# Performance work log

Hardware: AMD Instinct MI355X
Metric: run time of the kernel (lower is better)

Reference implementation:

```python
import jax, jax.numpy as jnp
import numpy as np

B, T, D = 2, 2048, 1024
HD = 128          # head_dim
NH = 16           # num_attention_heads
NKV = 8           # num_key_value_heads
EPS = 1e-6
ROPE_THETA = 1000000.0


def setup_inputs() -> dict:
    key = jax.random.key(0)
    ks = jax.random.split(key, 7)
    s = 0.02
    return {
        "x": jax.random.normal(ks[0], (B, T, D), dtype=jnp.float32),
        "wq": jax.random.normal(ks[1], (D, NH * HD), dtype=jnp.float32) * s,
        "wk": jax.random.normal(ks[2], (D, NKV * HD), dtype=jnp.float32) * s,
        "wv": jax.random.normal(ks[3], (D, NKV * HD), dtype=jnp.float32) * s,
        "wo": jax.random.normal(ks[4], (NH * HD, D), dtype=jnp.float32) * s,
        "q_norm_w": jnp.ones((HD,), dtype=jnp.float32),
        "k_norm_w": jnp.ones((HD,), dtype=jnp.float32),
    }


def _rms_norm(x, w):
    # torch source: x / (rms + eps) * w  (eps added OUTSIDE the sqrt)
    rms = jnp.sqrt(jnp.mean(x * x, axis=-1, keepdims=True))
    return w * (x / (rms + EPS))


def _rope_cos_sin(seq_len):
    pos = jnp.arange(seq_len, dtype=jnp.float32)
    thetas = ROPE_THETA ** (-2.0 * jnp.arange(HD // 2, dtype=jnp.float32) / HD)
    freqs = pos[:, None] * thetas[None, :]            # [T, HD//2]
    return jnp.cos(freqs), jnp.sin(freqs)


def _apply_rope(x, cos, sin):
    # x: [B, H, T, HD]; interleaved complex pairs (view_as_complex layout)
    xr = x[..., 0::2]
    xi = x[..., 1::2]
    c = cos[None, None, :, :]
    s = sin[None, None, :, :]
    out_r = xr * c - xi * s
    out_i = xr * s + xi * c
    return jnp.stack([out_r, out_i], axis=-1).reshape(x.shape)


def reference(x, wq, wk, wv, wo, q_norm_w, k_norm_w):
    b, t, d = x.shape
    q = (x @ wq).reshape(b, t, NH, HD).transpose(0, 2, 1, 3)    # [B,NH,T,HD]
    k = (x @ wk).reshape(b, t, NKV, HD).transpose(0, 2, 1, 3)   # [B,NKV,T,HD]
    v = (x @ wv).reshape(b, t, NKV, HD).transpose(0, 2, 1, 3)

    q = _rms_norm(q, q_norm_w)
    k = _rms_norm(k, k_norm_w)

    rep = NH // NKV
    k = jnp.repeat(k, rep, axis=1)   # GQA expand -> [B,NH,T,HD]
    v = jnp.repeat(v, rep, axis=1)

    cos, sin = _rope_cos_sin(t)
    q = _apply_rope(q, cos, sin)
    k = _apply_rope(k, cos, sin)

    scale = 1.0 / jnp.sqrt(jnp.float32(HD))
    scores = jnp.einsum("bhqd,bhkd->bhqk", q, k) * scale        # [B,NH,T,T]
    mask = jnp.triu(jnp.full((t, t), -jnp.inf, dtype=scores.dtype), k=1)
    scores = scores + mask
    attn = jax.nn.softmax(scores.astype(jnp.float32), axis=-1).astype(q.dtype)
    y = jnp.einsum("bhqk,bhkd->bhqd", attn, v)                  # [B,NH,T,HD]
    y = y.transpose(0, 2, 1, 3).reshape(b, t, NH * HD)
    return y @ wo
```

## Files before the change

kernel.cpp:

```cpp
#include <hip/hip_runtime.h>
#include <hip/hip_bf16.h>
#include <cstdint>
#include <cstddef>

using bf16 = __hip_bfloat16;
using short8 = __attribute__((ext_vector_type(8))) short;
using f32x4  = __attribute__((ext_vector_type(4))) float;
using f32x16 = __attribute__((ext_vector_type(16))) float;

#define DEVI __device__ __forceinline__

DEVI void async_ld16(const void* g, void* l) {
  __builtin_amdgcn_global_load_lds(
      (const __attribute__((address_space(1))) unsigned int*)g,
      (__attribute__((address_space(3))) unsigned int*)l, 16, 0, 0);
}

DEVI unsigned int cvt_pk_bf16(float lo, float hi) {
  unsigned int r;
  asm("v_cvt_pk_bf16_f32 %0, %1, %2" : "=v"(r) : "v"(lo), "v"(hi));
  return r;
}

__global__ void cvt_f32_bf16(const float* __restrict__ in, bf16* __restrict__ out, int n4) {
  int i = blockIdx.x * blockDim.x + threadIdx.x;
  if (i >= n4) return;
  float4 v = ((const float4*)in)[i];
  union { bf16 h[4]; ushort4 u; } o;
  o.h[0] = __float2bfloat16(v.x);
  o.h[1] = __float2bfloat16(v.y);
  o.h[2] = __float2bfloat16(v.z);
  o.h[3] = __float2bfloat16(v.w);
  ((ushort4*)out)[i] = o.u;
}

__global__ __launch_bounds__(256) void transpose_cvt(
    const float* __restrict__ in, bf16* __restrict__ out, int K, int N) {
  __shared__ float tile[32][33];
  int n0 = blockIdx.x * 32, k0 = blockIdx.y * 32;
  int tx = threadIdx.x & 31, ty = threadIdx.x >> 5;
#pragma unroll
  for (int i = 0; i < 32; i += 8)
    tile[ty + i][tx] = in[(size_t)(k0 + ty + i) * N + n0 + tx];
  __syncthreads();
#pragma unroll
  for (int i = 0; i < 32; i += 8)
    out[(size_t)(n0 + ty + i) * K + k0 + tx] = __float2bfloat16(tile[tx][ty + i]);
}

__global__ __launch_bounds__(256) void transpose_cvt3(
    const float* __restrict__ wq, const float* __restrict__ wk,
    const float* __restrict__ wv, bf16* __restrict__ wt) {
  __shared__ float tile[32][33];
  int z = blockIdx.z;
  const float* src; int N, coff, roff;
  if (z < 2)       { src = wq; N = 2048; coff = z * 1024; roff = z * 1024; }
  else if (z == 2) { src = wk; N = 1024; coff = 0;        roff = 2048; }
  else             { src = wv; N = 1024; coff = 0;        roff = 3072; }
  int n0 = coff + blockIdx.x * 32, k0 = blockIdx.y * 32;
  int tx = threadIdx.x & 31, ty = threadIdx.x >> 5;
#pragma unroll
  for (int i = 0; i < 32; i += 8)
    tile[ty + i][tx] = src[(size_t)(k0 + ty + i) * N + n0 + tx];
  __syncthreads();
#pragma unroll
  for (int i = 0; i < 32; i += 8)
    wt[(size_t)(roff + blockIdx.x * 32 + ty + i) * 1024 + k0 + tx] =
        __float2bfloat16(tile[tx][ty + i]);
}

__global__ void rope_tab(float2* __restrict__ tab) {
  int t = blockIdx.x, i = threadIdx.x;
  float ex = -2.f * (float)i * (1.f / 128.f);
  float theta = exp2f(ex * 19.9315685693241741f);
  float f = (float)t * theta;
  float sv, cv;
  sincosf(f, &sv, &cv);
  tab[t * 64 + i] = make_float2(cv, sv);
}

__global__ __launch_bounds__(256, 2) void gemm_qkv(
    const bf16* __restrict__ A, const bf16* __restrict__ Bt,
    const float* __restrict__ qnw, const float* __restrict__ knw,
    const float2* __restrict__ tab,
    bf16* __restrict__ Qh, bf16* __restrict__ Kh, bf16* __restrict__ Vt) {
  __shared__ alignas(16) bf16 As[2][128 * 64];
  __shared__ alignas(16) bf16 Bs[2][128 * 64];
  const int tid = threadIdx.x, lane = tid & 63, w = tid >> 6;
  const int wm = w >> 1, wn = w & 1;
  const int bx = blockIdx.x;
  const int m0 = blockIdx.y * 128, n0 = bx * 128;
  const int K = 1024, nt = 16;
  f32x4 acc[4][4] = {};

  const int srow = lane >> 3;
  const int scb  = (lane & 7) * 16;

  auto stage = [&](int buf, int kt) {
#pragma unroll
    for (int i = 0; i < 4; i++) {
      int row = w * 32 + i * 8 + srow;
      int src_cb = scb ^ ((row & 7) << 4);
      async_ld16((const char*)(A  + (size_t)(m0 + row) * K + kt * 64) + src_cb,
                 (char*)As[buf] + w * 4096 + i * 1024);
      async_ld16((const char*)(Bt + (size_t)(n0 + row) * K + kt * 64) + src_cb,
                 (char*)Bs[buf] + w * 4096 + i * 1024);
    }
  };

  stage(0, 0);
  stage(1, 1);

  for (int kt = 0; kt < nt; ++kt) {
    const int buf = kt & 1;
    if (kt + 1 < nt) asm volatile("s_waitcnt vmcnt(8)" ::: "memory");
    else             asm volatile("s_waitcnt vmcnt(0)" ::: "memory");
    __builtin_amdgcn_s_barrier();
#pragma unroll
    for (int ks = 0; ks < 2; ks++) {
      short8 af[4], bfr[4];
#pragma unroll
      for (int mi = 0; mi < 4; mi++) {
        int row = wm * 64 + mi * 16 + (lane & 15);
        int cb = (ks * 64 + (lane >> 4) * 16) ^ ((row & 7) << 4);
        af[mi] = *(const short8*)((const char*)As[buf] + row * 128 + cb);
      }
#pragma unroll
      for (int ni = 0; ni < 4; ni++) {
        int row = wn * 64 + ni * 16 + (lane & 15);
        int cb = (ks * 64 + (lane >> 4) * 16) ^ ((row & 7) << 4);
        bfr[ni] = *(const short8*)((const char*)Bs[buf] + row * 128 + cb);
      }
#pragma unroll
      for (int mi = 0; mi < 4; mi++)
#pragma unroll
        for (int ni = 0; ni < 4; ni++)
          acc[mi][ni] = __builtin_amdgcn_mfma_f32_16x16x32_bf16(af[mi], bfr[ni], acc[mi][ni], 0, 0, 0);
    }
    __builtin_amdgcn_s_barrier();
    __builtin_amdgcn_sched_barrier(0);
    if (kt + 2 < nt) stage(buf, kt + 2);
  }

  const int b = m0 >> 11;

  if (bx < 24) {
    __syncthreads();
    float* ssb = (float*)As;
    float s[4][4];
#pragma unroll
    for (int mi = 0; mi < 4; mi++)
#pragma unroll
      for (int r = 0; r < 4; r++) {
        float v0 = acc[mi][0][r], v1 = acc[mi][1][r];
        float v2 = acc[mi][2][r], v3 = acc[mi][3][r];
        float t = v0 * v0 + v1 * v1 + v2 * v2 + v3 * v3;
        t += __shfl_xor(t, 1);
        t += __shfl_xor(t, 2);
        t += __shfl_xor(t, 4);
        t += __shfl_xor(t, 8);
        s[mi][r] = t;
      }
    if ((lane & 15) == 0) {
#pragma unroll
      for (int mi = 0; mi < 4; mi++)
#pragma unroll
        for (int r = 0; r < 4; r++)
          ssb[wn * 128 + wm * 64 + mi * 16 + (lane >> 4) * 4 + r] = s[mi][r];
    }
    __syncthreads();

    const int isQ = (bx < 16);
    const int h = isQ ? bx : bx - 16;
    const float* wnp = isQ ? qnw : knw;
    bf16* dst = isQ ? Qh : Kh;
    const int NHH = isQ ? 16 : 8;
    const float qs = isQ ? 0.12751744416163417f : 1.f;
    float wd[4];
#pragma unroll
    for (int ni = 0; ni < 4; ni++) wd[ni] = wnp[wn * 64 + ni * 16 + (lane & 15)];

#pragma unroll
    for (int mi = 0; mi < 4; mi++)
#pragma unroll
      for (int r = 0; r < 4; r++) {
        int rl = wm * 64 + mi * 16 + (lane >> 4) * 4 + r;
        float tot = ssb[rl] + ssb[128 + rl];
        float inv = qs / (sqrtf(tot * 0.0078125f) + 1e-6f);
        int t = (m0 + rl) & 2047;
        bf16* drow = dst + ((size_t)(b * NHH + h) * 2048 + t) * 128;
#pragma unroll
        for (int ni = 0; ni < 4; ni++) {
          int d = wn * 64 + ni * 16 + (lane & 15);
          float val = acc[mi][ni][r] * inv * wd[ni];
          float prt = __shfl_xor(val, 1);
          float2 cs = tab[t * 64 + (d >> 1)];
          float o = (d & 1) ? (prt * cs.y + val * cs.x)
                            : (val * cs.x - prt * cs.y);
          drow[d] = __float2bfloat16(o);
        }
      }
  } else {
    __syncthreads();
    bf16* vt = (bf16*)As;
    const int vh = bx - 24;
#pragma unroll
    for (int mi = 0; mi < 4; mi++)
#pragma unroll
      for (int ni = 0; ni < 4; ni++) {
        int d = wn * 64 + ni * 16 + (lane & 15);
        int tl = wm * 64 + mi * 16 + (lane >> 4) * 4;
        unsigned int p0 = cvt_pk_bf16(acc[mi][ni][0], acc[mi][ni][1]);
        unsigned int p1 = cvt_pk_bf16(acc[mi][ni][2], acc[mi][ni][3]);
        int byte = d * 256 + ((tl * 2) ^ ((d & 7) << 4));
        *(uint2*)((char*)vt + byte) = make_uint2(p0, p1);
      }
    __syncthreads();
    bf16* dstV = Vt + (size_t)(b * 8 + vh) * 128 * 2048 + (m0 & 2047);
#pragma unroll
    for (int i = 0; i < 8; i++) {
      int flat = tid + i * 256;
      int d = flat >> 4, g = flat & 15;
      short8 v = *(const short8*)((const char*)vt + d * 256 + ((g * 16) ^ ((d & 7) << 4)));
      *(short8*)(dstV + (size_t)d * 2048 + g * 8) = v;
    }
  }
}

__global__ __launch_bounds__(256, 2) void gemm_out(
    const bf16* __restrict__ A, const bf16* __restrict__ Bt,
    float* __restrict__ C, int M, int N, int K) {
  __shared__ alignas(16) bf16 As[2][128 * 64];
  __shared__ alignas(16) bf16 Bs[2][128 * 64];
  const int tid = threadIdx.x, lane = tid & 63, w = tid >> 6;
  const int wm = w >> 1, wn = w & 1;
  const int m0 = blockIdx.y * 128, n0 = blockIdx.x * 128;
  const int nt = K >> 6;
  f32x4 acc[4][4] = {};

  const int srow = lane >> 3;
  const int scb  = (lane & 7) * 16;

  auto stage = [&](int buf, int kt) {
#pragma unroll
    for (int i = 0; i < 4; i++) {
      int row = w * 32 + i * 8 + srow;
      int src_cb = scb ^ ((row & 7) << 4);
      async_ld16((const char*)(A  + (size_t)(m0 + row) * K + kt * 64) + src_cb,
                 (char*)As[buf] + w * 4096 + i * 1024);
      async_ld16((const char*)(Bt + (size_t)(n0 + row) * K + kt * 64) + src_cb,
                 (char*)Bs[buf] + w * 4096 + i * 1024);
    }
  };

  stage(0, 0);
  stage(1, 1);

  for (int kt = 0; kt < nt; ++kt) {
    const int buf = kt & 1;
    if (kt + 1 < nt) asm volatile("s_waitcnt vmcnt(8)" ::: "memory");
    else             asm volatile("s_waitcnt vmcnt(0)" ::: "memory");
    __builtin_amdgcn_s_barrier();
#pragma unroll
    for (int ks = 0; ks < 2; ks++) {
      short8 af[4], bfr[4];
#pragma unroll
      for (int mi = 0; mi < 4; mi++) {
        int row = wm * 64 + mi * 16 + (lane & 15);
        int cb = (ks * 64 + (lane >> 4) * 16) ^ ((row & 7) << 4);
        af[mi] = *(const short8*)((const char*)As[buf] + row * 128 + cb);
      }
#pragma unroll
      for (int ni = 0; ni < 4; ni++) {
        int row = wn * 64 + ni * 16 + (lane & 15);
        int cb = (ks * 64 + (lane >> 4) * 16) ^ ((row & 7) << 4);
        bfr[ni] = *(const short8*)((const char*)Bs[buf] + row * 128 + cb);
      }
#pragma unroll
      for (int mi = 0; mi < 4; mi++)
#pragma unroll
        for (int ni = 0; ni < 4; ni++)
          acc[mi][ni] = __builtin_amdgcn_mfma_f32_16x16x32_bf16(af[mi], bfr[ni], acc[mi][ni], 0, 0, 0);
    }
    __builtin_amdgcn_s_barrier();
    __builtin_amdgcn_sched_barrier(0);
    if (kt + 2 < nt) stage(buf, kt + 2);
  }

  const int c0 = n0 + wn * 64 + (lane & 15);
  const int r0 = m0 + wm * 64 + (lane >> 4) * 4;
#pragma unroll
  for (int mi = 0; mi < 4; mi++)
#pragma unroll
    for (int ni = 0; ni < 4; ni++)
#pragma unroll
      for (int r = 0; r < 4; r++)
        C[(size_t)(r0 + mi * 16 + r) * N + (c0 + ni * 16)] = acc[mi][ni][r];
}

__global__ __launch_bounds__(512, 1) void flash_attn10(
    const bf16* __restrict__ Qh, const bf16* __restrict__ Kh,
    const bf16* __restrict__ Vt, bf16* __restrict__ Y) {
  __shared__ alignas(16) bf16 KB[4][64 * 128];
  __shared__ alignas(16) bf16 VB[4][128 * 64];
  __shared__ float MLs[128][2];
  const int tid = threadIdx.x, lane = tid & 63, w = tid >> 6;
  const int hi = lane >> 5, lq = lane & 31;
  const int grp = w >> 2, wl = w & 3;

  const int g = blockIdx.x;
  const int bh = (g & 7) * 4 + ((g >> 3) & 3);
  const int p  = g >> 5;
  const int b = bh >> 4, h = bh & 15, kvh = h >> 1;

  const bf16* Qg = Qh + (size_t)(b * 16 + h) * 2048 * 128;
  const bf16* Kg = Kh + (size_t)(b * 8 + kvh) * 2048 * 128;
  const bf16* Vg = Vt + (size_t)(b * 8 + kvh) * 128 * 2048;

  short8 qf[8];
  f32x16 oacc[4];
  float m, l;
  int qw = 0, qg = 0;

  auto stage2 = [&](int set, int k0e) {
#pragma unroll
    for (int gb = 0; gb < 2; gb++) {
      const int k0 = k0e + gb * 64;
      char* kb = (char*)KB[set * 2 + gb];
      char* vb = (char*)VB[set * 2 + gb];
#pragma unroll
      for (int i = 0; i < 2; i++) {
        int c = w * 2 + i;
        {
          int row = c * 4 + (lane >> 4);
          int cb = ((lane & 15) * 16) ^ ((row & 7) << 4);
          async_ld16((const char*)Kg + (size_t)(k0 + row) * 256 + cb, kb + c * 1024);
        }
        {
          int row = c * 8 + (lane >> 3);
          int cb = ((lane & 7) * 16) ^ ((row & 7) << 4);
          async_ld16((const char*)Vg + (size_t)row * 4096 + (size_t)k0 * 2 + cb, vb + c * 1024);
        }
      }
    }
  };

  auto setupTile = [&](int q0) {
    qw = q0 + wl * 32;
    qg = qw + lq;
#pragma unroll
    for (int dc = 0; dc < 8; dc++)
      qf[dc] = *(const short8*)(Qg + (size_t)qg * 128 + dc * 16 + hi * 8);
#pragma unroll
    for (int dc = 0; dc < 4; dc++)
#pragma unroll
      for (int r = 0; r < 16; r++) oacc[dc][r] = 0.f;
    m = -1e30f;
    l = 0.f;
  };

  auto computeStep = [&](int bufI, int k0) {
    f32x16 st[2] = {};
#pragma unroll
    for (int kc = 0; kc < 2; kc++) {
      int row = kc * 32 + lq;
      int swz = (row & 7) << 4;
      const char* kbase = (const char*)KB[bufI] + row * 256;
#pragma unroll
      for (int dc = 0; dc < 8; dc++) {
        short8 kf = *(const short8*)(kbase + ((dc * 32 + hi * 16) ^ swz));
        st[kc] = __builtin_amdgcn_mfma_f32_32x32x16_bf16(kf, qf[dc], st[kc], 0, 0, 0);
      }
    }
    const bool msk = (k0 + 63 > qw);
    if (msk) {
#pragma unroll
      for (int kc = 0; kc < 2; kc++)
#pragma unroll
        for (int rr = 0; rr < 16; rr++) {
          int kg = k0 + kc * 32 + (rr & 3) + 8 * (rr >> 2) + 4 * hi;
          if (kg > qg) st[kc][rr] = -1e30f;
        }
    }
    float mx[16];
#pragma unroll
    for (int rr = 0; rr < 16; rr++) mx[rr] = fmaxf(st[0][rr], st[1][rr]);
#pragma unroll
    for (int off = 8; off >= 1; off >>= 1)
#pragma unroll
      for (int rr = 0; rr < 8; rr++)
        if (rr < off) mx[rr] = fmaxf(mx[rr], mx[rr + off]);
    float pm = fmaxf(mx[0], __shfl_xor(mx[0], 32));
    if (__any(pm > m + 8.f)) {
      float mnew = fmaxf(m, pm);
      float alpha = exp2f(m - mnew);
      m = mnew;
      l *= alpha;
      float al[16];
#pragma unroll
      for (int rr = 0; rr < 16; rr++)
        al[rr] = __shfl(alpha, (rr & 3) + 8 * (rr >> 2) + 4 * hi);
#pragma unroll
      for (int dc = 0; dc < 4; dc++)
#pragma unroll
        for (int rr = 0; rr < 16; rr++) oacc[dc][rr] *= al[rr];
    }
#pragma unroll
    for (int kc = 0; kc < 2; kc++)
#pragma unroll
      for (int rr = 0; rr < 16; rr++) st[kc][rr] = exp2f(st[kc][rr] - m);
    float sm[16];
#pragma unroll
    for (int rr = 0; rr < 16; rr++) sm[rr] = st[0][rr] + st[1][rr];
#pragma unroll
    for (int off = 8; off >= 1; off >>= 1)
#pragma unroll
      for (int rr = 0; rr < 8; rr++)
        if (rr < off) sm[rr] += sm[rr + off];
    l += sm[0] + __shfl_xor(sm[0], 32);
    short8 af[4];
#pragma unroll
    for (int kc = 0; kc < 2; kc++)
#pragma unroll
      for (int sb = 0; sb < 2; sb++) {
        int base = sb * 8;
        unsigned int a01 = cvt_pk_bf16(st[kc][base + 0], st[kc][base + 1]);
        unsigned int a23 = cvt_pk_bf16(st[kc][base + 2], st[kc][base + 3]);
        unsigned int b01 = cvt_pk_bf16(st[kc][base + 4], st[kc][base + 5]);
        unsigned int b23 = cvt_pk_bf16(st[kc][base + 6], st[kc][base + 7]);
        unsigned int xa01 = (unsigned int)__shfl_xor((int)a01, 32);
        unsigned int xa23 = (unsigned int)__shfl_xor((int)a23, 32);
        unsigned int xb01 = (unsigned int)__shfl_xor((int)b01, 32);
        unsigned int xb23 = (unsigned int)__shfl_xor((int)b23, 32);
        union { unsigned int u[4]; short8 s; } f;
        f.u[0] = hi ? xb01 : a01;
        f.u[1] = hi ? xb23 : a23;
        f.u[2] = hi ? b01 : xa01;
        f.u[3] = hi ? b23 : xa23;
        af[kc * 2 + sb] = f.s;
      }
#pragma unroll
    for (int dc = 0; dc < 4; dc++) {
      int row = dc * 32 + lq;
      int swz = (row & 7) << 4;
      const char* vbase = (const char*)VB[bufI] + row * 128;
#pragma unroll
      for (int ks = 0; ks < 4; ks++) {
        short8 vf = *(const short8*)(vbase + ((ks * 32 + hi * 16) ^ swz));
        oacc[dc] = __builtin_amdgcn_mfma_f32_32x32x16_bf16(af[ks], vf, oacc[dc], 0, 0, 0);
      }
    }
  };

  auto runRounds = [&](int n) {
    const int R = n >> 1;
    for (int r = 0; r < R; ++r) {
      asm volatile("s_waitcnt vmcnt(0)" ::: "memory");
      __builtin_amdgcn_s_barrier();
      if (r + 1 < R) stage2((r + 1) & 1, (2 * r + 2) * 64);
      __builtin_amdgcn_sched_barrier(0);
      const int s = 2 * r + grp, k0 = s * 64;
      const int bufI = (r & 1) * 2 + grp;
      if (k0 < qw + 32) computeStep(bufI, k0);
    }
  };

  auto writePartials = [&]() {
    float* base = (wl < 2) ? (float*)KB[2] : (float*)VB[2];
#pragma unroll
    for (int dc = 0; dc < 4; dc++)
#pragma unroll
      for (int rr = 0; rr < 16; rr++) {
        int q = (wl & 1) * 32 + (rr & 3) + 8 * (rr >> 2) + 4 * hi;
        base[q * 128 + dc * 32 + lq] = oacc[dc][rr];
      }
    if (lane < 32) {
      MLs[wl * 32 + lane][0] = m;
      MLs[wl * 32 + lane][1] = l;
    }
  };

  auto mergeAndY = [&](int q0) {
    float m1 = MLs[wl * 32 + lq][0], l1 = MLs[wl * 32 + lq][1];
    float mN = fmaxf(m, m1);
    float e0 = exp2f(m - mN), e1 = exp2f(m1 - mN);
    float lT = l * e0 + l1 * e1;
    float inv = 1.f / lT;
    float e0r[16], e1r[16], ivr[16];
#pragma unroll
    for (int rr = 0; rr < 16; rr++) {
      int src = (rr & 3) + 8 * (rr >> 2) + 4 * hi;
      e0r[rr] = __shfl(e0, src);
      e1r[rr] = __shfl(e1, src);
      ivr[rr] = __shfl(inv, src);
    }
    const float* base = (wl < 2) ? (const float*)KB[2] : (const float*)VB[2];
#pragma unroll
    for (int dc = 0; dc < 4; dc++)
#pragma unroll
      for (int rr = 0; rr < 16; rr++) {
        int q = (wl & 1) * 32 + (rr & 3) + 8 * (rr >> 2) + 4 * hi;
        float o1 = base[q * 128 + dc * 32 + lq];
        float oT = oacc[dc][rr] * e0r[rr] + o1 * e1r[rr];
        int t = q0 + wl * 32 + (rr & 3) + 8 * (rr >> 2) + 4 * hi;
        Y[(size_t)(b * 2048 + t) * 2048 + h * 128 + dc * 32 + lq] =
            __float2bfloat16(oT * ivr[rr]);
      }
  };

  const int jA = 15 - p, jB = p;
  const int q0A = jA * 128, nA = 2 * jA + 2;
  const int q0B = jB * 128, nB = 2 * jB + 2;

  setupTile(q0A);
  stage2(0, 0);
  runRounds(nA);
  __syncthreads();
  stage2(0, 0);
  if (grp == 1) writePartials();
  __syncthreads();
  if (grp == 0) mergeAndY(q0A);
  setupTile(q0B);
  runRounds(nB);
  __syncthreads();
  if (grp == 1) writePartials();
  __syncthreads();
  if (grp == 0) mergeAndY(q0B);
}

extern "C" void kernel_launch(void* const* d_in, const int* in_sizes, int n_in,
                              void* d_out, int out_size, void* d_ws, size_t ws_size,
                              hipStream_t stream) {
  (void)in_sizes; (void)n_in; (void)out_size; (void)ws_size;
  const float* x   = (const float*)d_in[0];
  const float* wq  = (const float*)d_in[1];
  const float* wk  = (const float*)d_in[2];
  const float* wv  = (const float*)d_in[3];
  const float* wo  = (const float*)d_in[4];
  const float* qnw = (const float*)d_in[5];
  const float* knw = (const float*)d_in[6];
  float* out = (float*)d_out;
  char* ws = (char*)d_ws;
  const size_t MB = 1u << 20;
  bf16*   xb  = (bf16*)(ws + 0 * MB);
  bf16*   wt  = (bf16*)(ws + 8 * MB);
  bf16*   wot = (bf16*)(ws + 16 * MB);
  float2* tab = (float2*)(ws + 52 * MB);
  bf16*   Qh  = (bf16*)(ws + 53 * MB);
  bf16*   Kh  = (bf16*)(ws + 69 * MB);
  bf16*   Vtr = (bf16*)(ws + 77 * MB);
  bf16*   Yb  = (bf16*)(ws + 85 * MB);

  cvt_f32_bf16<<<4096, 256, 0, stream>>>(x, xb, 1048576);
  transpose_cvt3<<<dim3(32, 32, 4), 256, 0, stream>>>(wq, wk, wv, wt);
  transpose_cvt<<<dim3(32, 64), 256, 0, stream>>>(wo, wot, 2048, 1024);
  rope_tab<<<2048, 64, 0, stream>>>(tab);
  gemm_qkv<<<dim3(32, 32), 256, 0, stream>>>(xb, wt, qnw, knw, tab, Qh, Kh, Vtr);
  flash_attn10<<<256, 512, 0, stream>>>(Qh, Kh, Vtr, Yb);
  gemm_out<<<dim3(8, 32), 256, 0, stream>>>(Yb, wot, out, 4096, 1024, 2048);
}
```

Baseline: 166.6 us.

## Merge prep kernels into one launch and shrink output GEMM M-tile to 64

The four preprocessing kernels (x conversion, QKV weight transpose, Wo transpose, rope table) are combined into a single launch that branches on block index, removing launch gaps between small kernels. The output projection GEMM now uses 64x128 tiles with each wave covering 64x32, doubling the grid from 256 to 512 blocks on the device and allowing three blocks per CU. This improves CU occupancy for the small output GEMM at the cost of more redundant B-tile loads and lower per-wave arithmetic intensity.

```diff
diff --git a/kernel.cpp b/kernel.cpp
--- a/kernel.cpp
+++ b/kernel.cpp
@@ -22,61 +22,55 @@
   return r;
 }
 
-__global__ void cvt_f32_bf16(const float* __restrict__ in, bf16* __restrict__ out, int n4) {
-  int i = blockIdx.x * blockDim.x + threadIdx.x;
-  if (i >= n4) return;
-  float4 v = ((const float4*)in)[i];
-  union { bf16 h[4]; ushort4 u; } o;
-  o.h[0] = __float2bfloat16(v.x);
-  o.h[1] = __float2bfloat16(v.y);
-  o.h[2] = __float2bfloat16(v.z);
-  o.h[3] = __float2bfloat16(v.w);
-  ((ushort4*)out)[i] = o.u;
-}
-
-__global__ __launch_bounds__(256) void transpose_cvt(
-    const float* __restrict__ in, bf16* __restrict__ out, int K, int N) {
-  __shared__ float tile[32][33];
-  int n0 = blockIdx.x * 32, k0 = blockIdx.y * 32;
-  int tx = threadIdx.x & 31, ty = threadIdx.x >> 5;
-#pragma unroll
-  for (int i = 0; i < 32; i += 8)
-    tile[ty + i][tx] = in[(size_t)(k0 + ty + i) * N + n0 + tx];
-  __syncthreads();
-#pragma unroll
-  for (int i = 0; i < 32; i += 8)
-    out[(size_t)(n0 + ty + i) * K + k0 + tx] = __float2bfloat16(tile[tx][ty + i]);
-}
-
-__global__ __launch_bounds__(256) void transpose_cvt3(
-    const float* __restrict__ wq, const float* __restrict__ wk,
-    const float* __restrict__ wv, bf16* __restrict__ wt) {
-  __shared__ float tile[32][33];
-  int z = blockIdx.z;
-  const float* src; int N, coff, roff;
-  if (z < 2)       { src = wq; N = 2048; coff = z * 1024; roff = z * 1024; }
-  else if (z == 2) { src = wk; N = 1024; coff = 0;        roff = 2048; }
-  else             { src = wv; N = 1024; coff = 0;        roff = 3072; }
-  int n0 = coff + blockIdx.x * 32, k0 = blockIdx.y * 32;
-  int tx = threadIdx.x & 31, ty = threadIdx.x >> 5;
-#pragma unroll
-  for (int i = 0; i < 32; i += 8)
-    tile[ty + i][tx] = src[(size_t)(k0 + ty + i) * N + n0 + tx];
-  __syncthreads();
-#pragma unroll
-  for (int i = 0; i < 32; i += 8)
-    wt[(size_t)(roff + blockIdx.x * 32 + ty + i) * 1024 + k0 + tx] =
-        __float2bfloat16(tile[tx][ty + i]);
-}
-
-__global__ void rope_tab(float2* __restrict__ tab) {
-  int t = blockIdx.x, i = threadIdx.x;
-  float ex = -2.f * (float)i * (1.f / 128.f);
-  float theta = exp2f(ex * 19.9315685693241741f);
-  float f = (float)t * theta;
-  float sv, cv;
-  sincosf(f, &sv, &cv);
-  tab[t * 64 + i] = make_float2(cv, sv);
+__global__ __launch_bounds__(256) void prep(
+    const float* __restrict__ x, const float* __restrict__ wq,
+    const float* __restrict__ wk, const float* __restrict__ wv,
+    const float* __restrict__ wo, bf16* __restrict__ xb,
+    bf16* __restrict__ wt, bf16* __restrict__ wot, float2* __restrict__ tab) {
+  const int z = blockIdx.x, tid = threadIdx.x;
+  if (z < 4096) {
+    int i = z * 256 + tid;
+    float4 v = ((const float4*)x)[i];
+    union { bf16 h[4]; ushort4 u; } o;
+    o.h[0] = __float2bfloat16(v.x);
+    o.h[1] = __float2bfloat16(v.y);
+    o.h[2] = __float2bfloat16(v.z);
+    o.h[3] = __float2bfloat16(v.w);
+    ((ushort4*)xb)[i] = o.u;
+  } else if (z < 10240) {
+    __shared__ float tile[32][33];
+    const float* src; bf16* dst; int N, K, n0, k0, roff;
+    if (z < 8192) {
+      int z2 = z - 4096;
+      int xb_ = z2 & 31, yb = (z2 >> 5) & 31, zz = z2 >> 10;
+      if (zz < 2)       { src = wq; N = 2048; n0 = zz * 1024 + xb_ * 32; roff = zz * 1024 + xb_ * 32; }
+      else if (zz == 2) { src = wk; N = 1024; n0 = xb_ * 32; roff = 2048 + xb_ * 32; }
+      else              { src = wv; N = 1024; n0 = xb_ * 32; roff = 3072 + xb_ * 32; }
+      K = 1024; k0 = yb * 32; dst = wt;
+    } else {
+      int z3 = z - 8192;
+      int xb_ = z3 & 31, yb = z3 >> 5;
+      src = wo; N = 1024; K = 2048; n0 = xb_ * 32; k0 = yb * 32; roff = xb_ * 32;
+      dst = wot;
+    }
+    int tx = tid & 31, ty = tid >> 5;
+#pragma unroll
+    for (int i = 0; i < 32; i += 8)
+      tile[ty + i][tx] = src[(size_t)(k0 + ty + i) * N + n0 + tx];
+    __syncthreads();
+#pragma unroll
+    for (int i = 0; i < 32; i += 8)
+      dst[(size_t)(roff + ty + i) * K + k0 + tx] = __float2bfloat16(tile[tx][ty + i]);
+  } else {
+    int z4 = z - 10240;
+    int t = z4 * 4 + (tid >> 6), i = tid & 63;
+    float ex = -2.f * (float)i * (1.f / 128.f);
+    float theta = exp2f(ex * 19.9315685693241741f);
+    float f = (float)t * theta;
+    float sv, cv;
+    sincosf(f, &sv, &cv);
+    tab[t * 64 + i] = make_float2(cv, sv);
+  }
 }
 
 __global__ __launch_bounds__(256, 2) void gemm_qkv(
@@ -227,29 +221,32 @@
   }
 }
 
-__global__ __launch_bounds__(256, 2) void gemm_out(
+__global__ __launch_bounds__(256, 3) void gemm_out64(
     const bf16* __restrict__ A, const bf16* __restrict__ Bt,
     float* __restrict__ C, int M, int N, int K) {
-  __shared__ alignas(16) bf16 As[2][128 * 64];
+  __shared__ alignas(16) bf16 As[2][64 * 64];
   __shared__ alignas(16) bf16 Bs[2][128 * 64];
   const int tid = threadIdx.x, lane = tid & 63, w = tid >> 6;
-  const int wm = w >> 1, wn = w & 1;
-  const int m0 = blockIdx.y * 128, n0 = blockIdx.x * 128;
+  const int m0 = blockIdx.y * 64, n0 = blockIdx.x * 128;
   const int nt = K >> 6;
-  f32x4 acc[4][4] = {};
-
-  const int srow = lane >> 3;
-  const int scb  = (lane & 7) * 16;
+  f32x4 acc[4][2] = {};
 
   auto stage = [&](int buf, int kt) {
 #pragma unroll
+    for (int i = 0; i < 2; i++) {
+      int c = tid + i * 256;
+      int row = c >> 3;
+      int cb = ((c & 7) * 16) ^ ((row & 7) << 4);
+      async_ld16((const char*)(A + (size_t)(m0 + row) * K + kt * 64) + cb,
+                 (char*)As[buf] + i * 4096 + tid * 16);
+    }
+#pragma unroll
     for (int i = 0; i < 4; i++) {
-      int row = w * 32 + i * 8 + srow;
-      int src_cb = scb ^ ((row & 7) << 4);
-      async_ld16((const char*)(A  + (size_t)(m0 + row) * K + kt * 64) + src_cb,
-                 (char*)As[buf] + w * 4096 + i * 1024);
-      async_ld16((const char*)(Bt + (size_t)(n0 + row) * K + kt * 64) + src_cb,
-                 (char*)Bs[buf] + w * 4096 + i * 1024);
+      int c = tid + i * 256;
+      int row = c >> 3;
+      int cb = ((c & 7) * 16) ^ ((row & 7) << 4);
+      async_ld16((const char*)(Bt + (size_t)(n0 + row) * K + kt * 64) + cb,
+                 (char*)Bs[buf] + i * 4096 + tid * 16);
     }
   };
 
@@ -258,28 +255,28 @@
 
   for (int kt = 0; kt < nt; ++kt) {
     const int buf = kt & 1;
-    if (kt + 1 < nt) asm volatile("s_waitcnt vmcnt(8)" ::: "memory");
+    if (kt + 1 < nt) asm volatile("s_waitcnt vmcnt(6)" ::: "memory");
     else             asm volatile("s_waitcnt vmcnt(0)" ::: "memory");
     __builtin_amdgcn_s_barrier();
 #pragma unroll
     for (int ks = 0; ks < 2; ks++) {
-      short8 af[4], bfr[4];
+      short8 af[4], bfr[2];
 #pragma unroll
       for (int mi = 0; mi < 4; mi++) {
-        int row = wm * 64 + mi * 16 + (lane & 15);
+        int row = mi * 16 + (lane & 15);
         int cb = (ks * 64 + (lane >> 4) * 16) ^ ((row & 7) << 4);
         af[mi] = *(const short8*)((const char*)As[buf] + row * 128 + cb);
       }
 #pragma unroll
-      for (int ni = 0; ni < 4; ni++) {
-        int row = wn * 64 + ni * 16 + (lane & 15);
+      for (int ni = 0; ni < 2; ni++) {
+        int row = w * 32 + ni * 16 + (lane & 15);
         int cb = (ks * 64 + (lane >> 4) * 16) ^ ((row & 7) << 4);
         bfr[ni] = *(const short8*)((const char*)Bs[buf] + row * 128 + cb);
       }
 #pragma unroll
       for (int mi = 0; mi < 4; mi++)
 #pragma unroll
-        for (int ni = 0; ni < 4; ni++)
+        for (int ni = 0; ni < 2; ni++)
           acc[mi][ni] = __builtin_amdgcn_mfma_f32_16x16x32_bf16(af[mi], bfr[ni], acc[mi][ni], 0, 0, 0);
     }
     __builtin_amdgcn_s_barrier();
@@ -287,12 +284,12 @@
     if (kt + 2 < nt) stage(buf, kt + 2);
   }
 
-  const int c0 = n0 + wn * 64 + (lane & 15);
-  const int r0 = m0 + wm * 64 + (lane >> 4) * 4;
+  const int c0 = n0 + w * 32 + (lane & 15);
+  const int r0 = m0 + (lane >> 4) * 4;
 #pragma unroll
   for (int mi = 0; mi < 4; mi++)
 #pragma unroll
-    for (int ni = 0; ni < 4; ni++)
+    for (int ni = 0; ni < 2; ni++)
 #pragma unroll
       for (int r = 0; r < 4; r++)
         C[(size_t)(r0 + mi * 16 + r) * N + (c0 + ni * 16)] = acc[mi][ni][r];
@@ -551,11 +548,8 @@
   bf16*   Vtr = (bf16*)(ws + 77 * MB);
   bf16*   Yb  = (bf16*)(ws + 85 * MB);
 
-  cvt_f32_bf16<<<4096, 256, 0, stream>>>(x, xb, 1048576);
-  transpose_cvt3<<<dim3(32, 32, 4), 256, 0, stream>>>(wq, wk, wv, wt);
-  transpose_cvt<<<dim3(32, 64), 256, 0, stream>>>(wo, wot, 2048, 1024);
-  rope_tab<<<2048, 64, 0, stream>>>(tab);
+  prep<<<10752, 256, 0, stream>>>(x, wq, wk, wv, wo, xb, wt, wot, tab);
   gemm_qkv<<<dim3(32, 32), 256, 0, stream>>>(xb, wt, qnw, knw, tab, Qh, Kh, Vtr);
   flash_attn10<<<256, 512, 0, stream>>>(Qh, Kh, Vtr, Yb);
-  gemm_out<<<dim3(8, 32), 256, 0, stream>>>(Yb, wot, out, 4096, 1024, 2048);
-}
+  gemm_out64<<<dim3(8, 64), 256, 0, stream>>>(Yb, wot, out, 4096, 1024, 2048);
+}
```

After: 156.2 us (median of 3 runs). -6.3%, faster.
